# Kernel optimization log

Measured on AMD Instinct MI355X. Metric: run time of the kernel, lower is better.

Reference implementation:

```python
import jax, jax.numpy as jnp
import numpy as np

N, E, F, H, C, G = 100000, 1600000, 128, 64, 40, 2048


def setup_inputs() -> dict:
    key = jax.random.key(0)
    ks = jax.random.split(key, 8)
    x = jax.random.normal(ks[0], (N, F), dtype=jnp.float32)
    edge_index = jax.random.randint(ks[1], (2, E), 0, N, dtype=jnp.int64)
    batch = jnp.sort(jax.random.randint(ks[2], (N,), 0, G, dtype=jnp.int64))
    def glorot(k, shp):
        fan_in, fan_out = shp
        s = jnp.sqrt(2.0 / (fan_in + fan_out))
        return jax.random.normal(k, shp, dtype=jnp.float32) * s
    return {
        "x": x, "edge_index": edge_index, "batch": batch,
        "pre_w": glorot(ks[3], (F, H)), "pre_b": jnp.zeros((H,), jnp.float32),
        "c1_w": glorot(ks[4], (H, H)), "c1_b": jnp.zeros((H,), jnp.float32),
        "n1_g": jnp.ones((H,), jnp.float32), "n1_b": jnp.zeros((H,), jnp.float32),
        "c2_w": glorot(ks[5], (H, H)), "c2_b": jnp.zeros((H,), jnp.float32),
        "n2_g": jnp.ones((H,), jnp.float32), "n2_b": jnp.zeros((H,), jnp.float32),
        "post_w": glorot(ks[6], (H, C)), "post_b": jnp.zeros((C,), jnp.float32),
    }


def _gcn_conv(h, src, dst, deg_isqrt, W, b):
    # GCNConv with self-loops and symmetric D^{-1/2}(A+I)D^{-1/2} normalization.
    hw = h @ W                                        # [N, H]
    coef = deg_isqrt[src] * deg_isqrt[dst]            # [E]
    msg = hw[src] * coef[:, None]                     # gather + scale
    agg = jax.ops.segment_sum(msg, dst, num_segments=N)
    agg = agg + hw * (deg_isqrt * deg_isqrt)[:, None]  # self-loop term
    return agg + b


def _layer_norm(h, g, b, eps=1e-5):
    mu = jnp.mean(h, axis=-1, keepdims=True)
    var = jnp.mean(jnp.square(h - mu), axis=-1, keepdims=True)
    return (h - mu) * jax.lax.rsqrt(var + eps) * g + b


def reference(x, edge_index, batch, pre_w, pre_b, c1_w, c1_b, n1_g, n1_b,
              c2_w, c2_b, n2_g, n2_b, post_w, post_b):
    src, dst = edge_index[0], edge_index[1]
    ones = jnp.ones((E,), dtype=x.dtype)
    deg = jax.ops.segment_sum(ones, dst, num_segments=N) + 1.0  # +1 self-loop
    deg_isqrt = jax.lax.rsqrt(deg)

    h = x @ pre_w + pre_b                              # pre-process MLP
    h1 = jax.nn.relu(_layer_norm(_gcn_conv(h, src, dst, deg_isqrt, c1_w, c1_b), n1_g, n1_b))
    h2 = jax.nn.relu(_layer_norm(_gcn_conv(h1, src, dst, deg_isqrt, c2_w, c2_b), n2_g, n2_b))
    skip = h1 + h2                                     # sum of skip connections
    readout = jax.ops.segment_sum(skip, batch, num_segments=G)  # sum pooling
    return readout @ post_w + post_b                   # [G, C]
```

## Files before the change

### kernel.cpp

```cpp
#include <hip/hip_runtime.h>
#include <hip/hip_fp16.h>

#define NN 100000
#define NE 1600000
#define FIN 128
#define HD 64
#define CO 40
#define NG 2048
#define NSB 196
#define SCAP 9216
#define GCAP 13312
#define CHUNK 4096
#define NSCAT ((NE + CHUNK - 1) / CHUNK)

typedef _Float16 half8 __attribute__((ext_vector_type(8)));
typedef float floatx4 __attribute__((ext_vector_type(4)));

union RowU { float4 f4; __half2 h2[4]; };

__global__ __launch_bounds__(256) void setup_kernel(int* __restrict__ scur,
                                                    float* __restrict__ readout,
                                                    unsigned int* __restrict__ dummy,
                                                    const float* __restrict__ pre_w,
                                                    const float* __restrict__ pre_b,
                                                    const float* __restrict__ c1_w,
                                                    const float* __restrict__ c2_w,
                                                    _Float16* __restrict__ wth,
                                                    float* __restrict__ beff,
                                                    _Float16* __restrict__ wt2h) {
    int b = blockIdx.x;
    if (b < 512) {
        int gid = b * 256 + threadIdx.x;
        if (gid < NG * HD) readout[gid] = 0.0f;
        if (gid < NSB) scur[gid * 16] = gid * SCAP;
        if (gid < HD / 2) dummy[gid] = 0u;
        return;
    }
    b -= 512;
    if (b < 32) {
        int o = b * 256 + threadIdx.x;
        int r = o >> 6, c = o & 63;
        float acc = 0.0f;
#pragma unroll 8
        for (int k = 0; k < HD; k++) acc = fmaf(pre_w[r * HD + k], c1_w[k * HD + c], acc);
        wth[c * FIN + r] = (_Float16)acc;
    } else if (b == 32) {
        int c = threadIdx.x;
        if (c < HD) {
            float acc = 0.0f;
#pragma unroll 8
            for (int k = 0; k < HD; k++) acc = fmaf(pre_b[k], c1_w[k * HD + c], acc);
            beff[c] = acc;
        }
    } else {
        int o = (b - 33) * 256 + threadIdx.x;
        int r = o >> 6, c = o & 63;
        wt2h[c * HD + r] = (_Float16)c2_w[o];
    }
}

__global__ __launch_bounds__(1024) void scatter_super(const int* __restrict__ src,
                                                      const int* __restrict__ dst,
                                                      int* __restrict__ scur,
                                                      unsigned int* __restrict__ stmp) {
    __shared__ int hist[NSB];
    __shared__ int gbase[NSB];
    int tid = threadIdx.x;
    int e0 = blockIdx.x * CHUNK;
    int d[4], s[4];
    if (tid < NSB) hist[tid] = 0;
    __syncthreads();
#pragma unroll
    for (int r = 0; r < 4; r++) {
        int e = e0 + tid + r * 1024;
        d[r] = -1; s[r] = 0;
        if (e < NE) {
            d[r] = dst[e];
            s[r] = src[e];
            atomicAdd(&hist[d[r] >> 9], 1);
        }
    }
    __syncthreads();
    if (tid < NSB) {
        int c = hist[tid];
        gbase[tid] = (c > 0) ? atomicAdd(&scur[tid * 16], c) : 0;
        hist[tid] = 0;
    }
    __syncthreads();
#pragma unroll
    for (int r = 0; r < 4; r++) {
        if (d[r] >= 0) {
            int b = d[r] >> 9;
            int p = atomicAdd(&hist[b], 1);
            stmp[gbase[b] + p] = ((unsigned int)(d[r] & 511) << 17) | (unsigned int)s[r];
        }
    }
}

__global__ __launch_bounds__(1024) void group_sort(const int* __restrict__ scur,
                                                   const unsigned int* __restrict__ stmp,
                                                   unsigned int* __restrict__ ssrc,
                                                   int* __restrict__ offs,
                                                   int* __restrict__ degn,
                                                   float* __restrict__ di) {
    __shared__ int lh[512];
    __shared__ int sc[512];
    __shared__ int lcur[512];
    int g = blockIdx.x;
    int tid = threadIdx.x;
    int base = g * SCAP;
    int cnt = scur[g * 16] - base;
    if (tid < 512) lh[tid] = 0;
    __syncthreads();
    unsigned int uv[9];
#pragma unroll
    for (int r = 0; r < 9; r++) {
        int i = tid + r * 1024;
        uv[r] = 0xFFFFFFFFu;
        if (i < cnt) {
            uv[r] = stmp[base + i];
            atomicAdd(&lh[uv[r] >> 17], 1);
        }
    }
    __syncthreads();
    int h = 0, pd = 0;
    if (tid < 512) {
        h = lh[tid];
        pd = (h + 7) & ~7;
        sc[tid] = pd;
    }
    __syncthreads();
    for (int off = 1; off < 512; off <<= 1) {
        int v = 0;
        if (tid >= off && tid < 512) v = sc[tid - off];
        __syncthreads();
        if (tid < 512) sc[tid] += v;
        __syncthreads();
    }
    if (tid < 512) {
        int excl = sc[tid] - pd;
        lcur[tid] = excl;
        int node = g * 512 + tid;
        if (node < NN) {
            offs[node] = g * GCAP + excl;
            degn[node] = pd;
            di[node] = rsqrtf((float)h + 1.0f);
        }
        size_t gb = (size_t)g * GCAP;
        for (int q = h; q < pd; q++) ssrc[gb + excl + q] = (unsigned int)NN;
    }
    __syncthreads();
#pragma unroll
    for (int r = 0; r < 9; r++) {
        unsigned int u = uv[r];
        if (u != 0xFFFFFFFFu) {
            int dl = (int)(u >> 17);
            int pos = atomicAdd(&lcur[dl], 1);
            ssrc[(size_t)g * GCAP + pos] = u & 0x1FFFFu;
        }
    }
}

__global__ __launch_bounds__(256, 4) void gemm1_mfma(const float* __restrict__ x,
                                                     const _Float16* __restrict__ wt,
                                                     const float* __restrict__ beff,
                                                     const float* __restrict__ di,
                                                     __half* __restrict__ hws) {
    __shared__ _Float16 wS[64 * 136];
    int tid = threadIdx.x;
    for (int i = tid; i < 1024; i += 256) {
        int n = i >> 4, k0 = (i & 15) * 8;
        *(uint4*)&wS[n * 136 + k0] = ((const uint4*)wt)[i];
    }
    __syncthreads();
    int wv = tid >> 6, lane = tid & 63;
    int l15 = lane & 15, lg = lane >> 4;
    int rbase = blockIdx.x * 64 + wv * 16;
    if (rbase >= NN) return;
    half8 bf[4][4];
#pragma unroll
    for (int ks = 0; ks < 4; ks++)
#pragma unroll
        for (int ns = 0; ns < 4; ns++)
            bf[ks][ns] = *(const half8*)&wS[(ns * 16 + l15) * 136 + ks * 32 + lg * 8];
    floatx4 acc[4];
#pragma unroll
    for (int ns = 0; ns < 4; ns++) acc[ns] = (floatx4){0.f, 0.f, 0.f, 0.f};
    const float* xrow = x + (size_t)(rbase + l15) * FIN;
#pragma unroll
    for (int ks = 0; ks < 4; ks++) {
        float4 lo = *(const float4*)(xrow + ks * 32 + lg * 8);
        float4 hi = *(const float4*)(xrow + ks * 32 + lg * 8 + 4);
        half8 a;
        a[0] = (_Float16)lo.x; a[1] = (_Float16)lo.y; a[2] = (_Float16)lo.z; a[3] = (_Float16)lo.w;
        a[4] = (_Float16)hi.x; a[5] = (_Float16)hi.y; a[6] = (_Float16)hi.z; a[7] = (_Float16)hi.w;
#pragma unroll
        for (int ns = 0; ns < 4; ns++)
            acc[ns] = __builtin_amdgcn_mfma_f32_16x16x32_f16(a, bf[ks][ns], acc[ns], 0, 0, 0);
    }
    int r0 = rbase + lg * 4;
#pragma unroll
    for (int ns = 0; ns < 4; ns++) {
        float be = beff[ns * 16 + l15];
#pragma unroll
        for (int r = 0; r < 4; r++) {
            float dn = di[r0 + r];
            hws[(size_t)(r0 + r) * HD + ns * 16 + l15] = __float2half((acc[ns][r] + be) * dn);
        }
    }
}

__global__ __launch_bounds__(256, 4) void conv_gemm_mfma(const __half* __restrict__ hin,
                                                         const _Float16* __restrict__ wt2,
                                                         const float* __restrict__ di,
                                                         __half* __restrict__ hws) {
    __shared__ _Float16 wS[64 * 72];
    int tid = threadIdx.x;
    for (int i = tid; i < 512; i += 256) {
        int n = i >> 3, k0 = (i & 7) * 8;
        *(uint4*)&wS[n * 72 + k0] = ((const uint4*)wt2)[i];
    }
    __syncthreads();
    int wv = tid >> 6, lane = tid & 63;
    int l15 = lane & 15, lg = lane >> 4;
    int rbase = blockIdx.x * 64 + wv * 16;
    if (rbase >= NN) return;
    half8 bf[2][4];
#pragma unroll
    for (int ks = 0; ks < 2; ks++)
#pragma unroll
        for (int ns = 0; ns < 4; ns++)
            bf[ks][ns] = *(const half8*)&wS[(ns * 16 + l15) * 72 + ks * 32 + lg * 8];
    floatx4 acc[4];
#pragma unroll
    for (int ns = 0; ns < 4; ns++) acc[ns] = (floatx4){0.f, 0.f, 0.f, 0.f};
    const __half* hrow = hin + (size_t)(rbase + l15) * HD;
#pragma unroll
    for (int ks = 0; ks < 2; ks++) {
        half8 a = *(const half8*)(hrow + ks * 32 + lg * 8);
#pragma unroll
        for (int ns = 0; ns < 4; ns++)
            acc[ns] = __builtin_amdgcn_mfma_f32_16x16x32_f16(a, bf[ks][ns], acc[ns], 0, 0, 0);
    }
    int r0 = rbase + lg * 4;
#pragma unroll
    for (int ns = 0; ns < 4; ns++) {
#pragma unroll
        for (int r = 0; r < 4; r++) {
            float dn = di[r0 + r];
            hws[(size_t)(r0 + r) * HD + ns * 16 + l15] = __float2half(acc[ns][r] * dn);
        }
    }
}

__device__ __forceinline__ RowU ldrow(const __half* __restrict__ hws, unsigned int idx, int fp) {
    RowU r;
    r.f4 = ((const float4*)(hws + (size_t)idx * HD))[fp];
    return r;
}

#define LDA8(A, B) { u0 = ldrow(hws, (A).x, fp); u1 = ldrow(hws, (A).y, fp); \
                     u2 = ldrow(hws, (A).z, fp); u3 = ldrow(hws, (A).w, fp); \
                     u4 = ldrow(hws, (B).x, fp); u5 = ldrow(hws, (B).y, fp); \
                     u6 = ldrow(hws, (B).z, fp); u7 = ldrow(hws, (B).w, fp); }
#define LDB8(A, B) { v0 = ldrow(hws, (A).x, fp); v1 = ldrow(hws, (A).y, fp); \
                     v2 = ldrow(hws, (A).z, fp); v3 = ldrow(hws, (A).w, fp); \
                     v4 = ldrow(hws, (B).x, fp); v5 = ldrow(hws, (B).y, fp); \
                     v6 = ldrow(hws, (B).z, fp); v7 = ldrow(hws, (B).w, fp); }
#define ACC4(Q, U) { hacc[Q][0] = __hadd2(hacc[Q][0], (U).h2[0]); \
                     hacc[Q][1] = __hadd2(hacc[Q][1], (U).h2[1]); \
                     hacc[Q][2] = __hadd2(hacc[Q][2], (U).h2[2]); \
                     hacc[Q][3] = __hadd2(hacc[Q][3], (U).h2[3]); }
#define ACCA8() { ACC4(0, u0) ACC4(1, u1) ACC4(2, u2) ACC4(3, u3) \
                  ACC4(0, u4) ACC4(1, u5) ACC4(2, u6) ACC4(3, u7) }
#define ACCB8() { ACC4(0, v0) ACC4(1, v1) ACC4(2, v2) ACC4(3, v3) \
                  ACC4(0, v4) ACC4(1, v5) ACC4(2, v6) ACC4(3, v7) }

__device__ __forceinline__ void gather_node8(const int* __restrict__ offs,
                                             const int* __restrict__ pdeg,
                                             const unsigned int* __restrict__ ssrc,
                                             const __half* __restrict__ hws,
                                             int node, int fp, float acc[8]) {
    int i0 = offs[node];
    int deg = pdeg[node];
    const uint4* ip = (const uint4*)(ssrc + i0);
    __half2 hacc[4][4];
#pragma unroll
    for (int s = 0; s < 4; s++)
#pragma unroll
        for (int t = 0; t < 4; t++) hacc[s][t] = __floats2half2_rn(0.f, 0.f);
    {
        RowU sl = ldrow(hws, (unsigned int)node, fp);
#pragma unroll
        for (int t = 0; t < 4; t++) hacc[0][t] = sl.h2[t];
    }
    int nit = deg >> 3;
    if (nit > 0) {
        RowU u0, u1, u2, u3, u4, u5, u6, u7;
        RowU v0, v1, v2, v3, v4, v5, v6, v7;
        {
            uint4 a = ip[0], b = ip[1];
            LDA8(a, b);
        }
        int it = 1;
        for (; it + 1 < nit; it += 2) {
            uint4 a1 = ip[2 * it], b1 = ip[2 * it + 1];
            LDB8(a1, b1);
            ACCA8();
            uint4 a2 = ip[2 * it + 2], b2 = ip[2 * it + 3];
            LDA8(a2, b2);
            ACCB8();
        }
        if (it < nit) {
            uint4 a1 = ip[2 * it], b1 = ip[2 * it + 1];
            LDB8(a1, b1);
            ACCA8();
            ACCB8();
        } else {
            ACCA8();
        }
    }
#pragma unroll
    for (int t = 0; t < 4; t++) {
        float2 a = __half22float2(hacc[0][t]);
        float2 b = __half22float2(hacc[1][t]);
        float2 c = __half22float2(hacc[2][t]);
        float2 d = __half22float2(hacc[3][t]);
        acc[2 * t]     = (a.x + b.x) + (c.x + d.x);
        acc[2 * t + 1] = (a.y + b.y) + (c.y + d.y);
    }
}

__device__ __forceinline__ void ln8(float v[8], int fp,
                                    const float* __restrict__ g,
                                    const float* __restrict__ bb,
                                    float y[8]) {
    float su = 0.0f;
#pragma unroll
    for (int t = 0; t < 8; t++) su += v[t];
    su += __shfl_xor(su, 1, 64); su += __shfl_xor(su, 2, 64); su += __shfl_xor(su, 4, 64);
    float mu = su * (1.0f / HD);
    float q = 0.0f;
#pragma unroll
    for (int t = 0; t < 8; t++) { float d = v[t] - mu; q += d * d; }
    q += __shfl_xor(q, 1, 64); q += __shfl_xor(q, 2, 64); q += __shfl_xor(q, 4, 64);
    float rstd = rsqrtf(q * (1.0f / HD) + 1e-5f);
    float4 ga = ((const float4*)g)[fp * 2], gb = ((const float4*)g)[fp * 2 + 1];
    float4 ba = ((const float4*)bb)[fp * 2], bc = ((const float4*)bb)[fp * 2 + 1];
    float gv[8] = {ga.x, ga.y, ga.z, ga.w, gb.x, gb.y, gb.z, gb.w};
    float bv[8] = {ba.x, ba.y, ba.z, ba.w, bc.x, bc.y, bc.z, bc.w};
#pragma unroll
    for (int t = 0; t < 8; t++) y[t] = fmaxf((v[t] - mu) * rstd * gv[t] + bv[t], 0.0f);
}

__global__ __launch_bounds__(256, 4) void gather_ln(const int* __restrict__ offs,
                                                    const int* __restrict__ pdeg,
                                                    const unsigned int* __restrict__ ssrc,
                                                    const float* __restrict__ di,
                                                    const __half* __restrict__ hws,
                                                    const float* __restrict__ cb,
                                                    const float* __restrict__ g,
                                                    const float* __restrict__ bb,
                                                    __half* __restrict__ out) {
    int wv = threadIdx.x >> 6;
    int lane = threadIdx.x & 63;
    int fp = lane & 7, gg = lane >> 3;
    int node = blockIdx.x * 32 + wv * 8 + gg;
    float acc[8];
    gather_node8(offs, pdeg, ssrc, hws, node, fp, acc);
    float4 ca = ((const float4*)cb)[fp * 2], cc = ((const float4*)cb)[fp * 2 + 1];
    float cv[8] = {ca.x, ca.y, ca.z, ca.w, cc.x, cc.y, cc.z, cc.w};
    float dn = di[node];
    float v[8], y[8];
#pragma unroll
    for (int t = 0; t < 8; t++) v[t] = acc[t] * dn + cv[t];
    ln8(v, fp, g, bb, y);
    union U { float4 f4; __half2 h2[4]; } u;
#pragma unroll
    for (int t = 0; t < 4; t++) u.h2[t] = __floats2half2_rn(y[2 * t], y[2 * t + 1]);
    ((float4*)(out + (size_t)node * HD))[fp] = u.f4;
}

__global__ __launch_bounds__(256, 4) void gather_ln_pool(const int* __restrict__ offs,
                                                         const int* __restrict__ pdeg,
                                                         const unsigned int* __restrict__ ssrc,
                                                         const float* __restrict__ di,
                                                         const __half* __restrict__ hws,
                                                         const float* __restrict__ cb,
                                                         const float* __restrict__ g,
                                                         const float* __restrict__ bb,
                                                         const __half* __restrict__ h1,
                                                         const int* __restrict__ batch,
                                                         float* __restrict__ readout) {
    __shared__ float ls[32][65];
    __shared__ int lb[32];
    int wv = threadIdx.x >> 6;
    int lane = threadIdx.x & 63;
    int fp = lane & 7, gg = lane >> 3;
    int node = blockIdx.x * 32 + wv * 8 + gg;
    float acc[8];
    gather_node8(offs, pdeg, ssrc, hws, node, fp, acc);
    float4 ca = ((const float4*)cb)[fp * 2], cc = ((const float4*)cb)[fp * 2 + 1];
    float cv[8] = {ca.x, ca.y, ca.z, ca.w, cc.x, cc.y, cc.z, cc.w};
    float dn = di[node];
    float v[8], y[8];
#pragma unroll
    for (int t = 0; t < 8; t++) v[t] = acc[t] * dn + cv[t];
    ln8(v, fp, g, bb, y);
    union U { float4 f4; __half2 h2[4]; } u;
    u.f4 = ((const float4*)(h1 + (size_t)node * HD))[fp];
    int row = wv * 8 + gg;
#pragma unroll
    for (int t = 0; t < 4; t++) {
        float2 p = __half22float2(u.h2[t]);
        ls[row][fp * 8 + 2 * t]     = y[2 * t] + p.x;
        ls[row][fp * 8 + 2 * t + 1] = y[2 * t + 1] + p.y;
    }
    if (fp == 0) lb[row] = batch[node];
    int r0 = wv * 8;
    int bu = lb[r0];
    bool uni = true;
#pragma unroll
    for (int r = 1; r < 8; r++) uni = uni && (lb[r0 + r] == bu);
    int f = lane;
    if (uni) {
        float s2 = 0.0f;
#pragma unroll
        for (int r = 0; r < 8; r++) s2 += ls[r0 + r][f];
        atomicAdd(&readout[(size_t)bu * HD + f], s2);
    } else {
        float s2 = ls[r0][f];
        int bprev = lb[r0];
#pragma unroll
        for (int r = 1; r < 8; r++) {
            int bn = lb[r0 + r];
            if (bn == bprev) {
                s2 += ls[r0 + r][f];
            } else {
                atomicAdd(&readout[(size_t)bprev * HD + f], s2);
                s2 = ls[r0 + r][f];
                bprev = bn;
            }
        }
        atomicAdd(&readout[(size_t)bprev * HD + f], s2);
    }
}

__global__ __launch_bounds__(256) void out_gemm(const float* __restrict__ r,
                                                const float* __restrict__ w,
                                                const float* __restrict__ b,
                                                float* __restrict__ out) {
    __shared__ float lw[HD * CO];
    for (int i = threadIdx.x; i < HD * CO; i += 256) lw[i] = w[i];
    __syncthreads();
    int grp = blockIdx.x * 4 + (threadIdx.x >> 6);
    int c = threadIdx.x & 63;
    if (grp >= NG || c >= CO) return;
    const float* rr = r + (size_t)grp * HD;
    float acc = b[c];
#pragma unroll 8
    for (int k = 0; k < HD; k++) acc = fmaf(rr[k], lw[k * CO + c], acc);
    out[(size_t)grp * CO + c] = acc;
}

extern "C" void kernel_launch(void* const* d_in, const int* in_sizes, int n_in,
                              void* d_out, int out_size, void* d_ws, size_t ws_size,
                              hipStream_t stream) {
    const float* x      = (const float*)d_in[0];
    const int*   ei     = (const int*)d_in[1];
    const int*   batch  = (const int*)d_in[2];
    const float* pre_w  = (const float*)d_in[3];
    const float* pre_b  = (const float*)d_in[4];
    const float* c1_w   = (const float*)d_in[5];
    const float* c1_b   = (const float*)d_in[6];
    const float* n1_g   = (const float*)d_in[7];
    const float* n1_b   = (const float*)d_in[8];
    const float* c2_w   = (const float*)d_in[9];
    const float* c2_b   = (const float*)d_in[10];
    const float* n2_g   = (const float*)d_in[11];
    const float* n2_b   = (const float*)d_in[12];
    const float* post_w = (const float*)d_in[13];
    const float* post_b = (const float*)d_in[14];

    const int* src = ei;
    const int* dst = ei + NE;

    char* p = (char*)d_ws;
    int*          scur    = (int*)p;          p += (size_t)NSB * 16 * 4;
    int*          offs    = (int*)p;          p += (size_t)NN * 4;
    int*          degn    = (int*)p;          p += (size_t)NN * 4;
    float*        di      = (float*)p;        p += (size_t)NN * 4;
    _Float16*     wth     = (_Float16*)p;     p += (size_t)FIN * HD * 2;
    _Float16*     wt2h    = (_Float16*)p;     p += (size_t)HD * HD * 2;
    float*        beff    = (float*)p;        p += 256;
    unsigned int* stmp    = (unsigned int*)p; p += (size_t)NSB * SCAP * 4;
    unsigned int* ssrc    = (unsigned int*)p; p += (size_t)NSB * GCAP * 4;
    float*        readout = (float*)p;        p += (size_t)NG * HD * 4;
    __half*       hws     = (__half*)p;       p += (size_t)(NN + 8) * HD * 2;
    __half*       h1      = (__half*)p;       p += (size_t)NN * HD * 2;

    setup_kernel<<<561, 256, 0, stream>>>(scur, readout,
                                          (unsigned int*)(hws + (size_t)NN * HD),
                                          pre_w, pre_b, c1_w, c2_w, wth, beff, wt2h);

    scatter_super<<<NSCAT, 1024, 0, stream>>>(src, dst, scur, stmp);
    group_sort<<<NSB, 1024, 0, stream>>>(scur, stmp, ssrc, offs, degn, di);

    gemm1_mfma<<<(NN + 63) / 64, 256, 0, stream>>>(x, wth, beff, di, hws);
    gather_ln<<<NN / 32, 256, 0, stream>>>(offs, degn, ssrc, di, hws, c1_b, n1_g, n1_b, h1);

    conv_gemm_mfma<<<(NN + 63) / 64, 256, 0, stream>>>(h1, wt2h, di, hws);
    gather_ln_pool<<<NN / 32, 256, 0, stream>>>(offs, degn, ssrc, di, hws, c2_b, n2_g, n2_b, h1, batch, readout);

    out_gemm<<<(NG + 3) / 4, 256, 0, stream>>>(readout, post_w, post_b, (float*)d_out);
}
```

Baseline: 237.8 us.

## Fuse second-layer GEMM into first gather+LayerNorm kernel via LDS tile

The layer-1 gather/LayerNorm kernel now stages its 32 output rows in shared memory and runs the layer-2 64x64 MFMA GEMM right away, writing the scaled result into a new hws2 buffer. This removes the separate conv_gemm launch and its re-read of h1 from global memory. A second buffer is needed because the original hws is still being read by other blocks, and its padding rows are zeroed in setup. The cost is extra LDS use and a block barrier inside the gather kernel, which may lower occupancy.

Measured after the change: 229.3 us. 1.04x faster.

```diff
diff --git a/kernel.cpp b/kernel.cpp
--- a/kernel.cpp
+++ b/kernel.cpp
@@ -21,6 +21,7 @@
 __global__ __launch_bounds__(256) void setup_kernel(int* __restrict__ scur,
                                                     float* __restrict__ readout,
                                                     unsigned int* __restrict__ dummy,
+                                                    unsigned int* __restrict__ dummy2,
                                                     const float* __restrict__ pre_w,
                                                     const float* __restrict__ pre_b,
                                                     const float* __restrict__ c1_w,
@@ -33,7 +34,7 @@
         int gid = b * 256 + threadIdx.x;
         if (gid < NG * HD) readout[gid] = 0.0f;
         if (gid < NSB) scur[gid * 16] = gid * SCAP;
-        if (gid < HD / 2) dummy[gid] = 0u;
+        if (gid < HD / 2) { dummy[gid] = 0u; dummy2[gid] = 0u; }
         return;
     }
     b -= 512;
@@ -206,49 +207,6 @@
         for (int r = 0; r < 4; r++) {
             float dn = di[r0 + r];
             hws[(size_t)(r0 + r) * HD + ns * 16 + l15] = __float2half((acc[ns][r] + be) * dn);
-        }
-    }
-}
-
-__global__ __launch_bounds__(256, 4) void conv_gemm_mfma(const __half* __restrict__ hin,
-                                                         const _Float16* __restrict__ wt2,
-                                                         const float* __restrict__ di,
-                                                         __half* __restrict__ hws) {
-    __shared__ _Float16 wS[64 * 72];
-    int tid = threadIdx.x;
-    for (int i = tid; i < 512; i += 256) {
-        int n = i >> 3, k0 = (i & 7) * 8;
-        *(uint4*)&wS[n * 72 + k0] = ((const uint4*)wt2)[i];
-    }
-    __syncthreads();
-    int wv = tid >> 6, lane = tid & 63;
-    int l15 = lane & 15, lg = lane >> 4;
-    int rbase = blockIdx.x * 64 + wv * 16;
-    if (rbase >= NN) return;
-    half8 bf[2][4];
-#pragma unroll
-    for (int ks = 0; ks < 2; ks++)
-#pragma unroll
-        for (int ns = 0; ns < 4; ns++)
-            bf[ks][ns] = *(const half8*)&wS[(ns * 16 + l15) * 72 + ks * 32 + lg * 8];
-    floatx4 acc[4];
-#pragma unroll
-    for (int ns = 0; ns < 4; ns++) acc[ns] = (floatx4){0.f, 0.f, 0.f, 0.f};
-    const __half* hrow = hin + (size_t)(rbase + l15) * HD;
-#pragma unroll
-    for (int ks = 0; ks < 2; ks++) {
-        half8 a = *(const half8*)(hrow + ks * 32 + lg * 8);
-#pragma unroll
-        for (int ns = 0; ns < 4; ns++)
-            acc[ns] = __builtin_amdgcn_mfma_f32_16x16x32_f16(a, bf[ks][ns], acc[ns], 0, 0, 0);
-    }
-    int r0 = rbase + lg * 4;
-#pragma unroll
-    for (int ns = 0; ns < 4; ns++) {
-#pragma unroll
-        for (int r = 0; r < 4; r++) {
-            float dn = di[r0 + r];
-            hws[(size_t)(r0 + r) * HD + ns * 16 + l15] = __float2half(acc[ns][r] * dn);
         }
     }
 }
@@ -353,18 +311,28 @@
     for (int t = 0; t < 8; t++) y[t] = fmaxf((v[t] - mu) * rstd * gv[t] + bv[t], 0.0f);
 }
 
-__global__ __launch_bounds__(256, 4) void gather_ln(const int* __restrict__ offs,
-                                                    const int* __restrict__ pdeg,
-                                                    const unsigned int* __restrict__ ssrc,
-                                                    const float* __restrict__ di,
-                                                    const __half* __restrict__ hws,
-                                                    const float* __restrict__ cb,
-                                                    const float* __restrict__ g,
-                                                    const float* __restrict__ bb,
-                                                    __half* __restrict__ out) {
-    int wv = threadIdx.x >> 6;
-    int lane = threadIdx.x & 63;
+__global__ __launch_bounds__(256, 4) void gather_ln_conv(const int* __restrict__ offs,
+                                                         const int* __restrict__ pdeg,
+                                                         const unsigned int* __restrict__ ssrc,
+                                                         const float* __restrict__ di,
+                                                         const __half* __restrict__ hws,
+                                                         const float* __restrict__ cb,
+                                                         const float* __restrict__ g,
+                                                         const float* __restrict__ bb,
+                                                         const _Float16* __restrict__ wt2,
+                                                         __half* __restrict__ h1out,
+                                                         __half* __restrict__ hws2) {
+    __shared__ _Float16 wS2[64 * 72];
+    __shared__ _Float16 yS[32 * 80];
+    int tid = threadIdx.x;
+    for (int i = tid; i < 512; i += 256) {
+        int n = i >> 3, k0 = (i & 7) * 8;
+        *(uint4*)&wS2[n * 72 + k0] = ((const uint4*)wt2)[i];
+    }
+    int wv = tid >> 6;
+    int lane = tid & 63;
     int fp = lane & 7, gg = lane >> 3;
+    int l15 = lane & 15, lg = lane >> 4;
     int node = blockIdx.x * 32 + wv * 8 + gg;
     float acc[8];
     gather_node8(offs, pdeg, ssrc, hws, node, fp, acc);
@@ -378,7 +346,37 @@
     union U { float4 f4; __half2 h2[4]; } u;
 #pragma unroll
     for (int t = 0; t < 4; t++) u.h2[t] = __floats2half2_rn(y[2 * t], y[2 * t + 1]);
-    ((float4*)(out + (size_t)node * HD))[fp] = u.f4;
+    ((float4*)(h1out + (size_t)node * HD))[fp] = u.f4;
+    *(float4*)&yS[(wv * 8 + gg) * 80 + fp * 8] = u.f4;
+    __syncthreads();
+    int tile = wv & 1;
+    int nsb = (wv >> 1) * 2;
+    half8 bf2[2][2];
+#pragma unroll
+    for (int ks = 0; ks < 2; ks++)
+#pragma unroll
+        for (int n = 0; n < 2; n++)
+            bf2[ks][n] = *(const half8*)&wS2[((nsb + n) * 16 + l15) * 72 + ks * 32 + lg * 8];
+    floatx4 acc2[2];
+    acc2[0] = (floatx4){0.f, 0.f, 0.f, 0.f};
+    acc2[1] = (floatx4){0.f, 0.f, 0.f, 0.f};
+    const _Float16* yrow = &yS[(tile * 16 + l15) * 80];
+#pragma unroll
+    for (int ks = 0; ks < 2; ks++) {
+        half8 a = *(const half8*)(yrow + ks * 32 + lg * 8);
+#pragma unroll
+        for (int n = 0; n < 2; n++)
+            acc2[n] = __builtin_amdgcn_mfma_f32_16x16x32_f16(a, bf2[ks][n], acc2[n], 0, 0, 0);
+    }
+    int r0 = blockIdx.x * 32 + tile * 16 + lg * 4;
+#pragma unroll
+    for (int n = 0; n < 2; n++) {
+#pragma unroll
+        for (int r = 0; r < 4; r++) {
+            float d2 = di[r0 + r];
+            hws2[(size_t)(r0 + r) * HD + (nsb + n) * 16 + l15] = __float2half(acc2[n][r] * d2);
+        }
+    }
 }
 
 __global__ __launch_bounds__(256, 4) void gather_ln_pool(const int* __restrict__ offs,
@@ -497,20 +495,24 @@
     unsigned int* ssrc    = (unsigned int*)p; p += (size_t)NSB * GCAP * 4;
     float*        readout = (float*)p;        p += (size_t)NG * HD * 4;
     __half*       hws     = (__half*)p;       p += (size_t)(NN + 8) * HD * 2;
+    __half*       hws2    = (__half*)p;       p += (size_t)(NN + 8) * HD * 2;
     __half*       h1      = (__half*)p;       p += (size_t)NN * HD * 2;
 
     setup_kernel<<<561, 256, 0, stream>>>(scur, readout,
                                           (unsigned int*)(hws + (size_t)NN * HD),
+                                          (unsigned int*)(hws2 + (size_t)NN * HD),
                                           pre_w, pre_b, c1_w, c2_w, wth, beff, wt2h);
 
     scatter_super<<<NSCAT, 1024, 0, stream>>>(src, dst, scur, stmp);
     group_sort<<<NSB, 1024, 0, stream>>>(scur, stmp, ssrc, offs, degn, di);
 
     gemm1_mfma<<<(NN + 63) / 64, 256, 0, stream>>>(x, wth, beff, di, hws);
-    gather_ln<<<NN / 32, 256, 0, stream>>>(offs, degn, ssrc, di, hws, c1_b, n1_g, n1_b, h1);
-
-    conv_gemm_mfma<<<(NN + 63) / 64, 256, 0, stream>>>(h1, wt2h, di, hws);
-    gather_ln_pool<<<NN / 32, 256, 0, stream>>>(offs, degn, ssrc, di, hws, c2_b, n2_g, n2_b, h1, batch, readout);
+
+    gather_ln_conv<<<NN / 32, 256, 0, stream>>>(offs, degn, ssrc, di, hws,
+                                                c1_b, n1_g, n1_b, wt2h, h1, hws2);
+
+    gather_ln_pool<<<NN / 32, 256, 0, stream>>>(offs, degn, ssrc, di, hws2,
+                                                c2_b, n2_g, n2_b, h1, batch, readout);
 
     out_gemm<<<(NG + 3) / 4, 256, 0, stream>>>(readout, post_w, post_b, (float*)d_out);
 }
```
